# Kernel tuning notes

Measured on AMD Instinct MI355X. Metric: run time of the kernel, lower is better.

The kernel has to match this reference:

```python
import jax, jax.numpy as jnp
import numpy as np

B, S, H, NH = 2, 2048, 1024, 16
HD = H // NH
BASE = 10000.0


def _rotate_half(x):
    x1, x2 = x[..., : x.shape[-1] // 2], x[..., x.shape[-1] // 2 :]
    return jnp.concatenate((-x2, x1), axis=-1)


def setup_inputs() -> dict:
    key = jax.random.key(0)
    ks = jax.random.split(key, 6)
    hidden_states = jax.random.normal(ks[0], (B, S, H), jnp.float32)
    scale = 0.02
    wq = jax.random.normal(ks[1], (H, H), jnp.float32) * scale
    wk = jax.random.normal(ks[2], (H, H), jnp.float32) * scale
    wv = jax.random.normal(ks[3], (H, H), jnp.float32) * scale
    wo = jax.random.normal(ks[4], (H, H), jnp.float32) * scale
    # additive causal mask, shape (B, 1, S, S): 0 on/below diagonal, large negative above
    neg = jnp.finfo(jnp.float32).min
    causal = jnp.where(jnp.tril(jnp.ones((S, S), dtype=bool)), 0.0, neg).astype(jnp.float32)
    attention_mask = jnp.broadcast_to(causal[None, None], (B, 1, S, S))
    position_ids = jnp.broadcast_to(jnp.arange(S, dtype=jnp.int32)[None], (B, S))
    return {
        "hidden_states": hidden_states,
        "attention_mask": attention_mask,
        "wq": wq,
        "wk": wk,
        "wv": wv,
        "wo": wo,
        "position_ids": position_ids,
    }


def reference(hidden_states, attention_mask, wq, wk, wv, wo, position_ids):
    b, s, h = hidden_states.shape
    dtype = hidden_states.dtype

    def proj(x, w):  # torch Linear: y = x @ w.T, then split heads -> (b, nh, s, hd)
        y = jnp.einsum("bsh,oh->bso", x, w)
        return y.reshape(b, s, NH, HD).transpose(0, 2, 1, 3)

    q = proj(hidden_states, wq)
    k = proj(hidden_states, wk)
    v = proj(hidden_states, wv)

    # rotary cache (computed in fp32 like torch), gathered by position_ids
    inv_freq = 1.0 / (BASE ** (jnp.arange(0, HD, 2, dtype=jnp.float32) / HD))
    t = jnp.arange(s, dtype=jnp.float32)
    freqs = jnp.outer(t, inv_freq)                  # (s, hd/2)
    emb = jnp.concatenate((freqs, freqs), axis=-1)  # (s, hd)
    pos = jnp.clip(position_ids, 0, s - 1)
    cos = jnp.cos(emb).astype(dtype)[pos][:, None]  # (b, 1, s, hd)
    sin = jnp.sin(emb).astype(dtype)[pos][:, None]

    q = q * cos + _rotate_half(q) * sin
    k = k * cos + _rotate_half(k) * sin

    scores = jnp.einsum("bhqd,bhkd->bhqk", q, k) / jnp.sqrt(jnp.asarray(HD, dtype))
    scores = scores + attention_mask
    attn = jax.nn.softmax(scores.astype(jnp.float32), axis=-1).astype(dtype)
    out = jnp.einsum("bhqk,bhkd->bhqd", attn, v)    # (b, nh, s, hd)
    out = out.transpose(0, 2, 1, 3).reshape(b, s, h)
    return jnp.einsum("bso,ho->bsh", out, wo)
```

## Files before the change

kernel.cpp:

```cpp
#include <hip/hip_runtime.h>
#include <cstdint>
#include <cstddef>

typedef unsigned short u16;
typedef __bf16 bf16x8 __attribute__((ext_vector_type(8)));
typedef float f32x4 __attribute__((ext_vector_type(4)));

constexpr int SEQ = 2048;
constexpr int HID = 1024;
constexpr int NHEAD = 16;
constexpr int HDIM = 64;

typedef __attribute__((address_space(1))) void gvoid;
typedef __attribute__((address_space(3))) void lvoid;

__device__ __forceinline__ u16 f2bf(float f) {
  union { float f; unsigned u; } v;
  v.f = f;
  unsigned r = v.u + 0x7fffu + ((v.u >> 16) & 1u);
  return (u16)(r >> 16);
}
__device__ __forceinline__ u16 f2bf_trunc(float f) {
  union { float f; unsigned u; } v;
  v.f = f;
  return (u16)(v.u >> 16);
}

__device__ __forceinline__ f32x4 mfma16(bf16x8 a, bf16x8 b, f32x4 c) {
  return __builtin_amdgcn_mfma_f32_16x16x32_bf16(a, b, c, 0, 0, 0);
}

__device__ __forceinline__ int detect_f32(const unsigned* __restrict__ hs) {
  unsigned w = hs[threadIdx.x & 63];
  u16 lo = (u16)(w & 0xffffu);
  int e = (lo >> 7) & 0xff;
  bool inr = (e >= 100 && e <= 154);
  unsigned long long m = __ballot(inr);
  return (__popcll(m) >= 48) ? 0 : 1;
}

__global__ __launch_bounds__(256) void cvt_kernel(
    const void* s0, const void* s1, const void* s2, const void* s3, const void* s4,
    u16* __restrict__ d0, u16* __restrict__ dW,
    float* __restrict__ cosb, float* __restrict__ sinb) {
  int b = blockIdx.x;
  if (b >= 4096) {
    int idx = (b - 4096) * 256 + threadIdx.x;
    int s = idx >> 5;
    int i = idx & 31;
    float inv_freq = expf(-(float)(2 * i) * (9.210340371976184f / 64.0f));
    float ang = (float)s * inv_freq;
    float c = cosf(ang), sn = sinf(ang);
    cosb[s * 64 + i]      = c;
    cosb[s * 64 + i + 32] = c;
    sinb[s * 64 + i]      = sn;
    sinb[s * 64 + i + 32] = sn;
    return;
  }
  const int is_f32 = detect_f32((const unsigned*)s0);
  const void* s; u16* d; long base;
  if (b < 2048) { s = s0; d = d0; base = (long)b * 2048; }
  else {
    int bb = b - 2048;
    int w = bb >> 9;
    base = (long)(bb & 511) * 2048;
    s = (w == 0) ? s1 : (w == 1) ? s2 : (w == 2) ? s3 : s4;
    d = dW + (long)w * 1048576;
  }
  long idx = base + (long)threadIdx.x * 8;
  if (is_f32) {
    const float* sf = (const float*)s;
    float4 a = *(const float4*)(sf + idx);
    float4 c = *(const float4*)(sf + idx + 4);
    ushort4 p0, p1;
    p0.x = f2bf(a.x); p0.y = f2bf(a.y); p0.z = f2bf(a.z); p0.w = f2bf(a.w);
    p1.x = f2bf(c.x); p1.y = f2bf(c.y); p1.z = f2bf(c.z); p1.w = f2bf(c.w);
    *(ushort4*)(d + idx) = p0;
    *(ushort4*)(d + idx + 4) = p1;
  } else {
    const u16* su = (const u16*)s;
    *(uint4*)(d + idx) = *(const uint4*)(su + idx);
  }
}

__device__ __forceinline__ void gemm_mainloop_256(
    const u16* __restrict__ Ag, const u16* __restrict__ Bg,
    int row0, int col0, f32x4 acc[8][4]) {
  __shared__ __align__(16) u16 As[2][256 * 64];
  __shared__ __align__(16) u16 Bs[2][256 * 64];
  const int t = threadIdx.x;
  const int lane = t & 63, wave = t >> 6;
  const int l15 = lane & 15, quad = lane >> 4;
  const int wm = wave >> 2, wn = wave & 3;
  const int srow = lane >> 3;
  const int cs = ((lane & 7) ^ srow) * 8;
  const u16* aS = Ag + (size_t)(row0 + wave * 32 + srow) * 1024 + cs;
  const u16* bS = Bg + (size_t)(col0 + wave * 32 + srow) * 1024 + cs;
  const int swz0 = ((quad)     ^ (l15 & 7)) * 8;
  const int swz1 = ((4 + quad) ^ (l15 & 7)) * 8;

#define STAGE_A(bi, k0_) do {                                                    \
    _Pragma("unroll")                                                            \
    for (int j = 0; j < 4; j++)                                                  \
      __builtin_amdgcn_global_load_lds((gvoid*)(aS + (k0_) + j * 8192),          \
          (lvoid*)(&As[bi][0] + wave * 2048 + j * 512), 16, 0, 0);               \
  } while (0)
#define STAGE_B(bi, k0_) do {                                                    \
    _Pragma("unroll")                                                            \
    for (int j = 0; j < 4; j++)                                                  \
      __builtin_amdgcn_global_load_lds((gvoid*)(bS + (k0_) + j * 8192),          \
          (lvoid*)(&Bs[bi][0] + wave * 2048 + j * 512), 16, 0, 0);               \
  } while (0)
#define PBAR() do {                                                              \
    __builtin_amdgcn_sched_barrier(0);                                           \
    __builtin_amdgcn_s_barrier();                                                \
    __builtin_amdgcn_sched_barrier(0);                                           \
  } while (0)
#define READ_AF(QM) do {                                                         \
    _Pragma("unroll")                                                            \
    for (int mi = 0; mi < 4; mi++) {                                             \
      const u16* ap = Ab + (wm * 128 + (QM) * 64 + mi * 16 + l15) * 64;          \
      af[mi][0] = *(const bf16x8*)(ap + swz0);                                   \
      af[mi][1] = *(const bf16x8*)(ap + swz1);                                   \
    }                                                                            \
  } while (0)
#define READ_BF(NB) do {                                                         \
    _Pragma("unroll")                                                            \
    for (int nj = 0; nj < 2; nj++) {                                             \
      const u16* bp = Bb + (wn * 64 + ((NB) + nj) * 16 + l15) * 64;              \
      bfr[nj][0] = *(const bf16x8*)(bp + swz0);                                  \
      bfr[nj][1] = *(const bf16x8*)(bp + swz1);                                  \
    }                                                                            \
  } while (0)
#define MFMA_PH(QM, NB) do {                                                     \
    __builtin_amdgcn_s_setprio(1);                                               \
    _Pragma("unroll")                                                            \
    for (int mi = 0; mi < 4; mi++)                                               \
    _Pragma("unroll")                                                            \
    for (int nj = 0; nj < 2; nj++)                                               \
    _Pragma("unroll")                                                            \
    for (int kk = 0; kk < 2; kk++)                                               \
      acc[(QM) * 4 + mi][(NB) + nj] =                                            \
          mfma16(af[mi][kk], bfr[nj][kk], acc[(QM) * 4 + mi][(NB) + nj]);        \
    __builtin_amdgcn_s_setprio(0);                                               \
  } while (0)

  STAGE_A(0, 0);
  STAGE_B(0, 0);
  asm volatile("s_waitcnt vmcnt(0)" ::: "memory");
  PBAR();

  for (int kt = 0; kt < 16; ++kt) {
    const int cur = kt & 1;
    const u16* Ab = &As[cur][0];
    const u16* Bb = &Bs[cur][0];
    const bool pf = (kt + 1 < 16);
    bf16x8 af[4][2], bfr[2][2];
    READ_AF(0); READ_BF(0);
    if (pf) STAGE_A(cur ^ 1, (kt + 1) * 64);
    PBAR();
    MFMA_PH(0, 0);
    PBAR();
    READ_BF(2);
    if (pf) STAGE_B(cur ^ 1, (kt + 1) * 64);
    PBAR();
    MFMA_PH(0, 2);
    PBAR();
    READ_AF(1); READ_BF(0);
    PBAR();
    MFMA_PH(1, 0);
    PBAR();
    READ_BF(2);
    PBAR();
    MFMA_PH(1, 2);
    if (pf) asm volatile("s_waitcnt vmcnt(0)" ::: "memory");
    PBAR();
  }
#undef STAGE_A
#undef STAGE_B
#undef PBAR
#undef READ_AF
#undef READ_BF
#undef MFMA_PH
}

__global__ __launch_bounds__(512, 2) void qkv_kernel(
    const u16* __restrict__ X, const u16* __restrict__ Wcat,
    const int* __restrict__ pos_ids,
    const float* __restrict__ cosb, const float* __restrict__ sinb,
    u16* __restrict__ q_ws, u16* __restrict__ k_ws, u16* __restrict__ vt_ws) {
  const int row0 = blockIdx.x * 256;
  const int col0 = blockIdx.y * 256;
  f32x4 acc[8][4];
#pragma unroll
  for (int i = 0; i < 8; i++)
#pragma unroll
    for (int j = 0; j < 4; j++) acc[i][j] = f32x4{0.f, 0.f, 0.f, 0.f};

  gemm_mainloop_256(X, Wcat, row0, col0, acc);

  const int t = threadIdx.x;
  const int lane = t & 63, wave = t >> 6;
  const int l15 = lane & 15, quad = lane >> 4;
  const int wm = wave >> 2, wn = wave & 3;
  const int gr0 = row0 + wm * 128;
  const int gc0 = col0 + wn * 64;
  const int z = gc0 >> 10;
  const int nh = (gc0 >> 6) & 15;
  const float qscale = (z == 0) ? 0.18033688011112042f : 1.0f;

  if (z < 2) {
    u16* dst = (z == 0) ? q_ws : k_ws;
#pragma unroll
    for (int i = 0; i < 8; i++) {
#pragma unroll
      for (int r = 0; r < 4; r++) {
        int m = gr0 + i * 16 + quad * 4 + r;
        int b = m >> 11, s = m & 2047;
        int p = pos_ids[m];
        p = min(max(p, 0), SEQ - 1);
#pragma unroll
        for (int j = 0; j < 4; j++) {
          int d = j * 16 + l15;
          float c = cosb[p * 64 + d];
          float sn = sinb[p * 64 + d];
          float v = acc[i][j][r];
          float partner = acc[i][j ^ 2][r];
          float rot = (j < 2) ? -partner : partner;
          float o = (v * c + rot * sn) * qscale;
          dst[((size_t)((b * NHEAD + nh) * SEQ + s) << 6) + d] = f2bf(o);
        }
      }
    }
  } else {
#pragma unroll
    for (int i = 0; i < 8; i++) {
      int m_base = gr0 + i * 16 + quad * 4;
      int b = m_base >> 11, s = m_base & 2047;
#pragma unroll
      for (int j = 0; j < 4; j++) {
        int d = j * 16 + l15;
        ushort4 pk;
        pk.x = f2bf(acc[i][j][0]);
        pk.y = f2bf(acc[i][j][1]);
        pk.z = f2bf(acc[i][j][2]);
        pk.w = f2bf(acc[i][j][3]);
        *(ushort4*)(vt_ws + ((size_t)((b * NHEAD + nh) * 64 + d)) * SEQ + s) = pk;
      }
    }
  }
}

__global__ __launch_bounds__(256) void attn_kernel(
    const u16* __restrict__ q_ws, const u16* __restrict__ k_ws,
    const u16* __restrict__ vt_ws, u16* __restrict__ attn_ws) {
  const int b = blockIdx.z;
  const int qt = b ? blockIdx.x : 15 - blockIdx.x;
  const int nh = blockIdx.y;
  const int bh = b * NHEAD + nh;
  __shared__ __align__(16) u16 Ks[2][128 * 64];
  __shared__ __align__(16) u16 Vts[2][64 * 128];
  __shared__ __align__(16) u16 Pl[128 * 64];

  const int t = threadIdx.x;
  const int lane = t & 63, wave = t >> 6;
  const int l15 = lane & 15, quad = lane >> 4;
  const int l7 = l15 & 7;
  const int wq0 = qt * 128 + wave * 32;

  bf16x8 aq[2][2];
#pragma unroll
  for (int i = 0; i < 2; i++) {
    const u16* qb = q_ws + ((size_t)bh * SEQ + wq0 + i * 16 + l15) * 64;
    aq[i][0] = *(const bf16x8*)(qb + quad * 8);
    aq[i][1] = *(const bf16x8*)(qb + 32 + quad * 8);
  }

  f32x4 O[2][4];
  float lp[2];
#pragma unroll
  for (int i = 0; i < 2; i++) {
    lp[i] = 0.f;
#pragma unroll
    for (int n = 0; n < 4; n++) O[i][n] = f32x4{0.f, 0.f, 0.f, 0.f};
  }

  const int krl = lane >> 3;
  const int kcs = ((lane & 7) ^ (krl & 7)) * 8;
  const u16* kS = k_ws + (size_t)bh * SEQ * 64 + (size_t)(wave * 32 + krl) * 64 + kcs;
  const int vrl = lane >> 4;
  const int vc4 = lane & 15;
  const u16* vS = vt_ws + (size_t)bh * 64 * SEQ + (size_t)(wave * 16 + vrl) * SEQ;
  int vx[4];
#pragma unroll
  for (int j = 0; j < 4; j++) vx[j] = (vc4 ^ ((4 * j + vrl) & 15)) * 8;

#define STAGE_KV(bi, kt_) do {                                                     \
    const size_t koff_ = (size_t)(kt_) * 8192;                                     \
    _Pragma("unroll")                                                              \
    for (int j = 0; j < 4; j++) {                                                  \
      __builtin_amdgcn_global_load_lds((gvoid*)(kS + koff_ + j * 512),             \
          (lvoid*)(&Ks[bi][0] + wave * 2048 + j * 512), 16, 0, 0);                 \
      __builtin_amdgcn_global_load_lds(                                            \
          (gvoid*)(vS + (size_t)j * 4 * SEQ + (kt_) * 128 + vx[j]),                \
          (lvoid*)(&Vts[bi][0] + wave * 2048 + j * 512), 16, 0, 0);                \
    }                                                                              \
  } while (0)

  const int nkt = qt + 1;
  STAGE_KV(0, 0);
  int cur = 0;
  for (int kt = 0; kt < nkt; ++kt) {
    if (kt + 1 < nkt) {
      STAGE_KV(cur ^ 1, kt + 1);
      asm volatile("s_waitcnt vmcnt(8)" ::: "memory");
    } else {
      asm volatile("s_waitcnt vmcnt(0)" ::: "memory");
    }
    __builtin_amdgcn_sched_barrier(0);
    __builtin_amdgcn_s_barrier();
    __builtin_amdgcn_sched_barrier(0);
    const u16* Ksb = &Ks[cur][0];
    const u16* Vtb = &Vts[cur][0];

#pragma unroll
    for (int h = 0; h < 2; h++) {
      f32x4 sc[2][4];
      __builtin_amdgcn_s_setprio(1);
#pragma unroll
      for (int ct = 0; ct < 4; ct++) {
        const u16* krow = Ksb + (h * 64 + ct * 16 + l15) * 64;
        bf16x8 bk0 = *(const bf16x8*)(krow + (quad ^ l7) * 8);
        bf16x8 bk1 = *(const bf16x8*)(krow + ((4 + quad) ^ l7) * 8);
#pragma unroll
        for (int i = 0; i < 2; i++) {
          f32x4 z = f32x4{0.f, 0.f, 0.f, 0.f};
          z = mfma16(bk0, aq[i][0], z);
          z = mfma16(bk1, aq[i][1], z);
          sc[i][ct] = z;
        }
      }
      __builtin_amdgcn_s_setprio(0);

      const int kbase = kt * 128 + h * 64;
      if (kt == qt) {
#pragma unroll
        for (int i = 0; i < 2; i++) {
          const int qrow = wq0 + i * 16 + l15;
          const int prow = (wave * 32 + i * 16 + l15) * 64;
#pragma unroll
          for (int ct = 0; ct < 4; ct++) {
            const int key0 = kbase + ct * 16 + quad * 4;
            float p[4];
#pragma unroll
            for (int r = 0; r < 4; r++) {
              float e = __builtin_amdgcn_exp2f(sc[i][ct][r]);
              if (key0 + r > qrow) e = 0.f;
              p[r] = e;
            }
            lp[i] += (p[0] + p[1]) + (p[2] + p[3]);
            ushort4 pk;
            pk.x = f2bf_trunc(p[0]); pk.y = f2bf_trunc(p[1]);
            pk.z = f2bf_trunc(p[2]); pk.w = f2bf_trunc(p[3]);
            *(ushort4*)&Pl[prow + ((ct * 2 + (quad >> 1)) ^ l7) * 8 + (quad & 1) * 4] = pk;
          }
        }
      } else {
#pragma unroll
        for (int i = 0; i < 2; i++) {
          const int prow = (wave * 32 + i * 16 + l15) * 64;
#pragma unroll
          for (int ct = 0; ct < 4; ct++) {
            float p[4];
#pragma unroll
            for (int r = 0; r < 4; r++) p[r] = __builtin_amdgcn_exp2f(sc[i][ct][r]);
            lp[i] += (p[0] + p[1]) + (p[2] + p[3]);
            ushort4 pk;
            pk.x = f2bf_trunc(p[0]); pk.y = f2bf_trunc(p[1]);
            pk.z = f2bf_trunc(p[2]); pk.w = f2bf_trunc(p[3]);
            *(ushort4*)&Pl[prow + ((ct * 2 + (quad >> 1)) ^ l7) * 8 + (quad & 1) * 4] = pk;
          }
        }
      }

      bf16x8 pa[2][2];
#pragma unroll
      for (int i = 0; i < 2; i++) {
        const u16* prow = Pl + (wave * 32 + i * 16 + l15) * 64;
        pa[i][0] = *(const bf16x8*)(prow + (quad ^ l7) * 8);
        pa[i][1] = *(const bf16x8*)(prow + ((4 + quad) ^ l7) * 8);
      }
      __builtin_amdgcn_s_setprio(1);
#pragma unroll
      for (int n = 0; n < 4; n++) {
        const u16* vrow = Vtb + (n * 16 + l15) * 128;
        bf16x8 bv0 = *(const bf16x8*)(vrow + ((h * 8 + quad) ^ l15) * 8);
        bf16x8 bv1 = *(const bf16x8*)(vrow + ((h * 8 + 4 + quad) ^ l15) * 8);
#pragma unroll
        for (int i = 0; i < 2; i++) {
          O[i][n] = mfma16(pa[i][0], bv0, O[i][n]);
          O[i][n] = mfma16(pa[i][1], bv1, O[i][n]);
        }
      }
      __builtin_amdgcn_s_setprio(0);
    }

    __builtin_amdgcn_sched_barrier(0);
    __builtin_amdgcn_s_barrier();
    __builtin_amdgcn_sched_barrier(0);
    cur ^= 1;
  }
#undef STAGE_KV

#pragma unroll
  for (int i = 0; i < 2; i++) {
    float l = lp[i];
    l += __shfl_xor(l, 16, 64);
    l += __shfl_xor(l, 32, 64);
#pragma unroll
    for (int r = 0; r < 4; r++) {
      float inv = 1.0f / __shfl(l, quad * 4 + r, 64);
      int q = wq0 + i * 16 + quad * 4 + r;
      size_t base = ((size_t)(b * SEQ + q)) * HID + nh * 64;
#pragma unroll
      for (int n = 0; n < 4; n++)
        attn_ws[base + n * 16 + l15] = f2bf(O[i][n][r] * inv);
    }
  }
}

__global__ __launch_bounds__(256) void out_proj_kernel(
    const u16* __restrict__ A, const u16* __restrict__ Wo, void* __restrict__ out,
    const unsigned* __restrict__ hs_raw) {
  __shared__ __align__(16) u16 As[2][64 * 64];
  __shared__ __align__(16) u16 Bs[2][128 * 64];
  const int row0 = blockIdx.x * 64;
  const int col0 = blockIdx.y * 128;
  const int is_f32 = detect_f32(hs_raw);
  const int t = threadIdx.x;
  const int lane = t & 63, wave = t >> 6;
  const int l15 = lane & 15, quad = lane >> 4;
  const int wm = wave >> 1, wn = wave & 1;
  const int cs = ((lane & 7) ^ ((lane >> 3) & 7)) * 8;
  const u16* aS = A  + (size_t)(row0 + wave * 16 + (lane >> 3)) * 1024 + cs;
  const u16* bS = Wo + (size_t)(col0 + wave * 32 + (lane >> 3)) * 1024 + cs;
  const int swz0 = ((quad)     ^ (l15 & 7)) * 8;
  const int swz1 = ((4 + quad) ^ (l15 & 7)) * 8;

  f32x4 acc[2][4];
#pragma unroll
  for (int i = 0; i < 2; i++)
#pragma unroll
    for (int j = 0; j < 4; j++) acc[i][j] = f32x4{0.f, 0.f, 0.f, 0.f};

#define STAGE_OP(bi, k0_) do {                                                   \
    _Pragma("unroll")                                                            \
    for (int j = 0; j < 2; j++)                                                  \
      __builtin_amdgcn_global_load_lds((gvoid*)(aS + (k0_) + j * 8192),          \
          (lvoid*)(&As[bi][0] + wave * 1024 + j * 512), 16, 0, 0);               \
    _Pragma("unroll")                                                            \
    for (int j = 0; j < 4; j++)                                                  \
      __builtin_amdgcn_global_load_lds((gvoid*)(bS + (k0_) + j * 8192),          \
          (lvoid*)(&Bs[bi][0] + wave * 2048 + j * 512), 16, 0, 0);               \
  } while (0)

  STAGE_OP(0, 0);
  int cur = 0;
  for (int k0 = 0; k0 < 1024; k0 += 64) {
    if (k0 + 64 < 1024) {
      STAGE_OP(cur ^ 1, k0 + 64);
      asm volatile("s_waitcnt vmcnt(6)" ::: "memory");
    } else {
      asm volatile("s_waitcnt vmcnt(0)" ::: "memory");
    }
    __builtin_amdgcn_sched_barrier(0);
    __builtin_amdgcn_s_barrier();
    __builtin_amdgcn_sched_barrier(0);
    const u16* Asb = &As[cur][0];
    const u16* Bsb = &Bs[cur][0];
#pragma unroll
    for (int kk = 0; kk < 2; kk++) {
      const int sw = kk ? swz1 : swz0;
      bf16x8 af[2], bfr[4];
#pragma unroll
      for (int i = 0; i < 2; i++)
        af[i] = *(const bf16x8*)(Asb + (wm * 32 + i * 16 + l15) * 64 + sw);
#pragma unroll
      for (int j = 0; j < 4; j++)
        bfr[j] = *(const bf16x8*)(Bsb + (wn * 64 + j * 16 + l15) * 64 + sw);
#pragma unroll
      for (int i = 0; i < 2; i++)
#pragma unroll
        for (int j = 0; j < 4; j++)
          acc[i][j] = mfma16(af[i], bfr[j], acc[i][j]);
    }
    __builtin_amdgcn_sched_barrier(0);
    __builtin_amdgcn_s_barrier();
    __builtin_amdgcn_sched_barrier(0);
    cur ^= 1;
  }
#undef STAGE_OP

  const int gr0 = row0 + wm * 32;
  const int gc0 = col0 + wn * 64;
#pragma unroll
  for (int i = 0; i < 2; i++)
#pragma unroll
    for (int r = 0; r < 4; r++) {
      int m = gr0 + i * 16 + quad * 4 + r;
      if (is_f32) {
        float* o = (float*)out;
#pragma unroll
        for (int j = 0; j < 4; j++)
          o[(size_t)m * 1024 + gc0 + j * 16 + l15] = acc[i][j][r];
      } else {
        u16* o = (u16*)out;
#pragma unroll
        for (int j = 0; j < 4; j++)
          o[(size_t)m * 1024 + gc0 + j * 16 + l15] = f2bf(acc[i][j][r]);
      }
    }
}

extern "C" void kernel_launch(void* const* d_in, const int* in_sizes, int n_in,
                              void* d_out, int out_size, void* d_ws, size_t ws_size,
                              hipStream_t stream) {
  const void* hs = d_in[0];
  const void* wq = d_in[2];
  const void* wk = d_in[3];
  const void* wv = d_in[4];
  const void* wo = d_in[5];
  const int* pos = (const int*)d_in[6];

  char* ws = (char*)d_ws;
  float* cosb = (float*)ws;
  float* sinb = (float*)(ws + (512 << 10));
  u16* xbf    = (u16*)(ws + (1 << 20));
  u16* wcat   = xbf + (size_t)4194304;
  u16* q_ws   = wcat + (size_t)4 * 1048576;
  u16* k_ws   = q_ws + (size_t)2 * NHEAD * SEQ * HDIM;
  u16* vt_ws  = k_ws + (size_t)2 * NHEAD * SEQ * HDIM;
  u16* attn_ws = vt_ws + (size_t)2 * NHEAD * SEQ * HDIM;

  cvt_kernel<<<4352, 256, 0, stream>>>(hs, wq, wk, wv, wo, xbf, wcat, cosb, sinb);
  qkv_kernel<<<dim3(16, 12), 512, 0, stream>>>(xbf, wcat, pos, cosb, sinb,
                                               q_ws, k_ws, vt_ws);
  attn_kernel<<<dim3(16, NHEAD, 2), 256, 0, stream>>>(q_ws, k_ws, vt_ws, attn_ws);
  out_proj_kernel<<<dim3(64, 8), 256, 0, stream>>>(attn_ws, wcat + (size_t)3 * 1048576,
                                                   d_out, (const unsigned*)hs);
}
```

Baseline: 195.4 us.

## Merge four kernels into two cooperative launches with grid-wide sync

Folds the conversion and QKV projection into one kernel, and attention and output projection into another. Each pair is separated by a cooperative-groups grid sync instead of a kernel boundary, and each falls back to two separate launches if the cooperative launch fails. The conversion now uses a grid-stride loop over the 192×512 QKV grid. Attention and out-proj share one static LDS buffer, and out-proj remaps its 64×8 tiles onto the 512 attention blocks. This aims to cut launch gaps and tail bubbles. The risks are grid-sync cost, residency limits on the cooperative grid, and reduced cvt parallelism.

After: 309.1 us. 58.2% more time.

```diff
diff --git a/kernel.cpp b/kernel.cpp
--- a/kernel.cpp
+++ b/kernel.cpp
@@ -1,6 +1,9 @@
 #include <hip/hip_runtime.h>
+#include <hip/hip_cooperative_groups.h>
 #include <cstdint>
 #include <cstddef>
+
+namespace cg = cooperative_groups;
 
 typedef unsigned short u16;
 typedef __bf16 bf16x8 __attribute__((ext_vector_type(8)));
@@ -39,47 +42,49 @@
   return (__popcll(m) >= 48) ? 0 : 1;
 }
 
-__global__ __launch_bounds__(256) void cvt_kernel(
+__device__ __forceinline__ void cvt_stage(
     const void* s0, const void* s1, const void* s2, const void* s3, const void* s4,
     u16* __restrict__ d0, u16* __restrict__ dW,
     float* __restrict__ cosb, float* __restrict__ sinb) {
-  int b = blockIdx.x;
-  if (b >= 4096) {
-    int idx = (b - 4096) * 256 + threadIdx.x;
-    int s = idx >> 5;
+  const int NT = 192 * 512;
+  const int flatb = blockIdx.y * gridDim.x + blockIdx.x;
+  const int gtid = flatb * 512 + threadIdx.x;
+  const int is_f32 = detect_f32((const unsigned*)s0);
+  for (long c = gtid; c < 1048576; c += NT) {
+    long idx = c << 3;
+    const void* s; u16* d; long off;
+    if (idx < 4194304) { s = s0; d = d0; off = idx; }
+    else {
+      long wi = idx - 4194304;
+      int w = (int)(wi >> 20);
+      off = wi & 1048575;
+      s = (w == 0) ? s1 : (w == 1) ? s2 : (w == 2) ? s3 : s4;
+      d = dW + ((long)w << 20);
+    }
+    if (is_f32) {
+      const float* sf = (const float*)s;
+      float4 a = *(const float4*)(sf + off);
+      float4 cc = *(const float4*)(sf + off + 4);
+      ushort4 p0, p1;
+      p0.x = f2bf(a.x); p0.y = f2bf(a.y); p0.z = f2bf(a.z); p0.w = f2bf(a.w);
+      p1.x = f2bf(cc.x); p1.y = f2bf(cc.y); p1.z = f2bf(cc.z); p1.w = f2bf(cc.w);
+      *(ushort4*)(d + off) = p0;
+      *(ushort4*)(d + off + 4) = p1;
+    } else {
+      const u16* su = (const u16*)s;
+      *(uint4*)(d + off) = *(const uint4*)(su + off);
+    }
+  }
+  for (int idx = gtid; idx < 65536; idx += NT) {
+    int srow = idx >> 5;
     int i = idx & 31;
     float inv_freq = expf(-(float)(2 * i) * (9.210340371976184f / 64.0f));
-    float ang = (float)s * inv_freq;
+    float ang = (float)srow * inv_freq;
     float c = cosf(ang), sn = sinf(ang);
-    cosb[s * 64 + i]      = c;
-    cosb[s * 64 + i + 32] = c;
-    sinb[s * 64 + i]      = sn;
-    sinb[s * 64 + i + 32] = sn;
-    return;
-  }
-  const int is_f32 = detect_f32((const unsigned*)s0);
-  const void* s; u16* d; long base;
-  if (b < 2048) { s = s0; d = d0; base = (long)b * 2048; }
-  else {
-    int bb = b - 2048;
-    int w = bb >> 9;
-    base = (long)(bb & 511) * 2048;
-    s = (w == 0) ? s1 : (w == 1) ? s2 : (w == 2) ? s3 : s4;
-    d = dW + (long)w * 1048576;
-  }
-  long idx = base + (long)threadIdx.x * 8;
-  if (is_f32) {
-    const float* sf = (const float*)s;
-    float4 a = *(const float4*)(sf + idx);
-    float4 c = *(const float4*)(sf + idx + 4);
-    ushort4 p0, p1;
-    p0.x = f2bf(a.x); p0.y = f2bf(a.y); p0.z = f2bf(a.z); p0.w = f2bf(a.w);
-    p1.x = f2bf(c.x); p1.y = f2bf(c.y); p1.z = f2bf(c.z); p1.w = f2bf(c.w);
-    *(ushort4*)(d + idx) = p0;
-    *(ushort4*)(d + idx + 4) = p1;
-  } else {
-    const u16* su = (const u16*)s;
-    *(uint4*)(d + idx) = *(const uint4*)(su + idx);
+    cosb[srow * 64 + i]      = c;
+    cosb[srow * 64 + i + 32] = c;
+    sinb[srow * 64 + i]      = sn;
+    sinb[srow * 64 + i + 32] = sn;
   }
 }
 
@@ -184,7 +189,7 @@
 #undef MFMA_PH
 }
 
-__global__ __launch_bounds__(512, 2) void qkv_kernel(
+__device__ __forceinline__ void qkv_stage(
     const u16* __restrict__ X, const u16* __restrict__ Wcat,
     const int* __restrict__ pos_ids,
     const float* __restrict__ cosb, const float* __restrict__ sinb,
@@ -251,16 +256,17 @@
   }
 }
 
-__global__ __launch_bounds__(256) void attn_kernel(
+__device__ __forceinline__ void attn_stage(
+    u16* __restrict__ smem,
     const u16* __restrict__ q_ws, const u16* __restrict__ k_ws,
     const u16* __restrict__ vt_ws, u16* __restrict__ attn_ws) {
+  u16* KsB  = smem;
+  u16* VtsB = smem + 16384;
+  u16* Pl   = smem + 32768;
   const int b = blockIdx.z;
   const int qt = b ? blockIdx.x : 15 - blockIdx.x;
   const int nh = blockIdx.y;
   const int bh = b * NHEAD + nh;
-  __shared__ __align__(16) u16 Ks[2][128 * 64];
-  __shared__ __align__(16) u16 Vts[2][64 * 128];
-  __shared__ __align__(16) u16 Pl[128 * 64];
 
   const int t = threadIdx.x;
   const int lane = t & 63, wave = t >> 6;
@@ -300,10 +306,10 @@
     _Pragma("unroll")                                                              \
     for (int j = 0; j < 4; j++) {                                                  \
       __builtin_amdgcn_global_load_lds((gvoid*)(kS + koff_ + j * 512),             \
-          (lvoid*)(&Ks[bi][0] + wave * 2048 + j * 512), 16, 0, 0);                 \
+          (lvoid*)(KsB + (bi) * 8192 + wave * 2048 + j * 512), 16, 0, 0);          \
       __builtin_amdgcn_global_load_lds(                                            \
           (gvoid*)(vS + (size_t)j * 4 * SEQ + (kt_) * 128 + vx[j]),                \
-          (lvoid*)(&Vts[bi][0] + wave * 2048 + j * 512), 16, 0, 0);                \
+          (lvoid*)(VtsB + (bi) * 8192 + wave * 2048 + j * 512), 16, 0, 0);         \
     }                                                                              \
   } while (0)
 
@@ -320,8 +326,8 @@
     __builtin_amdgcn_sched_barrier(0);
     __builtin_amdgcn_s_barrier();
     __builtin_amdgcn_sched_barrier(0);
-    const u16* Ksb = &Ks[cur][0];
-    const u16* Vtb = &Vts[cur][0];
+    const u16* Ksb = KsB + cur * 8192;
+    const u16* Vtb = VtsB + cur * 8192;
 
 #pragma unroll
     for (int h = 0; h < 2; h++) {
@@ -429,13 +435,15 @@
   }
 }
 
-__global__ __launch_bounds__(256) void out_proj_kernel(
+__device__ __forceinline__ void outproj_stage(
+    u16* __restrict__ smem,
     const u16* __restrict__ A, const u16* __restrict__ Wo, void* __restrict__ out,
     const unsigned* __restrict__ hs_raw) {
-  __shared__ __align__(16) u16 As[2][64 * 64];
-  __shared__ __align__(16) u16 Bs[2][128 * 64];
-  const int row0 = blockIdx.x * 64;
-  const int col0 = blockIdx.y * 128;
+  u16* AsB = smem;
+  u16* BsB = smem + 8192;
+  const int flat = (blockIdx.z * gridDim.y + blockIdx.y) * gridDim.x + blockIdx.x;
+  const int row0 = (flat >> 3) * 64;
+  const int col0 = (flat & 7) * 128;
   const int is_f32 = detect_f32(hs_raw);
   const int t = threadIdx.x;
   const int lane = t & 63, wave = t >> 6;
@@ -457,11 +465,11 @@
     _Pragma("unroll")                                                            \
     for (int j = 0; j < 2; j++)                                                  \
       __builtin_amdgcn_global_load_lds((gvoid*)(aS + (k0_) + j * 8192),          \
-          (lvoid*)(&As[bi][0] + wave * 1024 + j * 512), 16, 0, 0);               \
+          (lvoid*)(AsB + (bi) * 4096 + wave * 1024 + j * 512), 16, 0, 0);        \
     _Pragma("unroll")                                                            \
     for (int j = 0; j < 4; j++)                                                  \
       __builtin_amdgcn_global_load_lds((gvoid*)(bS + (k0_) + j * 8192),          \
-          (lvoid*)(&Bs[bi][0] + wave * 2048 + j * 512), 16, 0, 0);               \
+          (lvoid*)(BsB + (bi) * 8192 + wave * 2048 + j * 512), 16, 0, 0);        \
   } while (0)
 
   STAGE_OP(0, 0);
@@ -476,8 +484,8 @@
     __builtin_amdgcn_sched_barrier(0);
     __builtin_amdgcn_s_barrier();
     __builtin_amdgcn_sched_barrier(0);
-    const u16* Asb = &As[cur][0];
-    const u16* Bsb = &Bs[cur][0];
+    const u16* Asb = AsB + cur * 4096;
+    const u16* Bsb = BsB + cur * 8192;
 #pragma unroll
     for (int kk = 0; kk < 2; kk++) {
       const int sw = kk ? swz1 : swz0;
@@ -520,6 +528,36 @@
           o[(size_t)m * 1024 + gc0 + j * 16 + l15] = f2bf(acc[i][j][r]);
       }
     }
+}
+
+template<int STAGE>
+__global__ __launch_bounds__(512, 2) void cvtqkv_kernel(
+    const void* hs, const void* wq, const void* wk, const void* wv, const void* wo,
+    u16* __restrict__ xbf, u16* __restrict__ wcat,
+    float* __restrict__ cosb, float* __restrict__ sinb,
+    const int* __restrict__ pos,
+    u16* __restrict__ q_ws, u16* __restrict__ k_ws, u16* __restrict__ vt_ws) {
+  if constexpr (STAGE != 2)
+    cvt_stage(hs, wq, wk, wv, wo, xbf, wcat, cosb, sinb);
+  if constexpr (STAGE == 0)
+    cg::this_grid().sync();
+  if constexpr (STAGE != 1)
+    qkv_stage(xbf, wcat, pos, cosb, sinb, q_ws, k_ws, vt_ws);
+}
+
+template<int STAGE>
+__global__ __launch_bounds__(256, 2) void attnop_kernel(
+    const u16* __restrict__ q_ws, const u16* __restrict__ k_ws,
+    const u16* __restrict__ vt_ws, u16* __restrict__ attn_ws,
+    const u16* __restrict__ Wo, void* __restrict__ out,
+    const unsigned* __restrict__ hs_raw) {
+  __shared__ __align__(16) u16 smem[40960];
+  if constexpr (STAGE != 2)
+    attn_stage(smem, q_ws, k_ws, vt_ws, attn_ws);
+  if constexpr (STAGE == 0)
+    cg::this_grid().sync();
+  if constexpr (STAGE != 1)
+    outproj_stage(smem, attn_ws, Wo, out, hs_raw);
 }
 
 extern "C" void kernel_launch(void* const* d_in, const int* in_sizes, int n_in,
@@ -541,11 +579,37 @@
   u16* k_ws   = q_ws + (size_t)2 * NHEAD * SEQ * HDIM;
   u16* vt_ws  = k_ws + (size_t)2 * NHEAD * SEQ * HDIM;
   u16* attn_ws = vt_ws + (size_t)2 * NHEAD * SEQ * HDIM;
-
-  cvt_kernel<<<4352, 256, 0, stream>>>(hs, wq, wk, wv, wo, xbf, wcat, cosb, sinb);
-  qkv_kernel<<<dim3(16, 12), 512, 0, stream>>>(xbf, wcat, pos, cosb, sinb,
-                                               q_ws, k_ws, vt_ws);
-  attn_kernel<<<dim3(16, NHEAD, 2), 256, 0, stream>>>(q_ws, k_ws, vt_ws, attn_ws);
-  out_proj_kernel<<<dim3(64, 8), 256, 0, stream>>>(attn_ws, wcat + (size_t)3 * 1048576,
-                                                   d_out, (const unsigned*)hs);
-}
+  const u16* Wo_bf = wcat + (size_t)3 * 1048576;
+  const unsigned* hs_raw = (const unsigned*)hs;
+  void* out = d_out;
+
+  {
+    void* args[13] = {(void*)&hs, (void*)&wq, (void*)&wk, (void*)&wv, (void*)&wo,
+                      (void*)&xbf, (void*)&wcat, (void*)&cosb, (void*)&sinb,
+                      (void*)&pos, (void*)&q_ws, (void*)&k_ws, (void*)&vt_ws};
+    hipError_t e = hipLaunchCooperativeKernel(
+        reinterpret_cast<const void*>(&cvtqkv_kernel<0>),
+        dim3(16, 12, 1), dim3(512, 1, 1), args, 0, stream);
+    if (e != hipSuccess) {
+      (void)hipGetLastError();
+      cvtqkv_kernel<1><<<dim3(16, 12), 512, 0, stream>>>(
+          hs, wq, wk, wv, wo, xbf, wcat, cosb, sinb, pos, q_ws, k_ws, vt_ws);
+      cvtqkv_kernel<2><<<dim3(16, 12), 512, 0, stream>>>(
+          hs, wq, wk, wv, wo, xbf, wcat, cosb, sinb, pos, q_ws, k_ws, vt_ws);
+    }
+  }
+  {
+    void* args[7] = {(void*)&q_ws, (void*)&k_ws, (void*)&vt_ws, (void*)&attn_ws,
+                     (void*)&Wo_bf, (void*)&out, (void*)&hs_raw};
+    hipError_t e = hipLaunchCooperativeKernel(
+        reinterpret_cast<const void*>(&attnop_kernel<0>),
+        dim3(16, 16, 2), dim3(256, 1, 1), args, 0, stream);
+    if (e != hipSuccess) {
+      (void)hipGetLastError();
+      attnop_kernel<1><<<dim3(16, 16, 2), 256, 0, stream>>>(
+          q_ws, k_ws, vt_ws, attn_ws, Wo_bf, out, hs_raw);
+      attnop_kernel<2><<<dim3(16, 16, 2), 256, 0, stream>>>(
+          q_ws, k_ws, vt_ws, attn_ws, Wo_bf, out, hs_raw);
+    }
+  }
+}
```
